# Performance work log

Measured on AMD Instinct MI355X. Metric: run time of the kernel, lower is better.

The kernel has to match this reference:

```python
import jax, jax.numpy as jnp
import numpy as np

N_NODES = 20000
N_EDGES = 320000
NUM_FEATURES = 128
CUTOFF = 5.0
NUM_RBF = 20
EPS = 1e-8


def setup_inputs() -> dict:
    key = jax.random.key(0)
    ks = jax.random.split(key, 10)
    v = jax.random.normal(ks[0], (N_NODES, NUM_FEATURES, 3), dtype=jnp.float32)
    s = jax.random.normal(ks[1], (N_NODES, NUM_FEATURES), dtype=jnp.float32)
    # edge list: col0 = src idx, col1 = dst idx (js), cols 2:5 = displacement vector
    src = jax.random.randint(ks[2], (N_EDGES,), 0, N_NODES).astype(jnp.float32)
    dst = jax.random.randint(ks[3], (N_EDGES,), 0, N_NODES).astype(jnp.float32)
    vec = jax.random.normal(ks[4], (N_EDGES, 3), dtype=jnp.float32) * 2.0
    r = jnp.concatenate([src[:, None], dst[:, None], vec], axis=1)
    # s_path params (torch Linear weight [out,in] -> stored here as [in,out])
    W1 = jax.random.normal(ks[5], (NUM_FEATURES, NUM_FEATURES), dtype=jnp.float32) * np.sqrt(2.0 / NUM_FEATURES)
    b1 = jnp.zeros((NUM_FEATURES,), dtype=jnp.float32)
    W2 = jax.random.normal(ks[6], (NUM_FEATURES, 3 * NUM_FEATURES), dtype=jnp.float32) * np.sqrt(2.0 / NUM_FEATURES)
    b2 = jnp.zeros((3 * NUM_FEATURES,), dtype=jnp.float32)
    # r_path params
    Wr = jax.random.normal(ks[7], (NUM_RBF, 3 * NUM_FEATURES), dtype=jnp.float32) * np.sqrt(1.0 / NUM_RBF)
    br = jnp.zeros((3 * NUM_FEATURES,), dtype=jnp.float32)
    return {"v": v, "s": s, "r": r, "W1": W1, "b1": b1, "W2": W2, "b2": b2, "Wr": Wr, "br": br}


def reference(v, s, r, W1, b1, W2, b2, Wr, br):
    nf = NUM_FEATURES
    js = r[:, 1].astype(jnp.int32)          # [E] destination node indices
    rv = r[:, 2:]                            # [E,3] displacement vectors

    # s_path: Linear -> SiLU -> Linear, computed per-node then gathered
    h = s @ W1 + b1
    phi = (h * jax.nn.sigmoid(h)) @ W2 + b2  # [N, 3*nf]

    # RBF expansion of edge distances
    norm_r = jnp.linalg.norm(rv, axis=1, keepdims=True)          # [E,1]
    norm_c = jnp.clip(norm_r, EPS)
    n = jnp.arange(1, NUM_RBF + 1, dtype=rv.dtype)[None, :]      # [1,20]
    rbf = jnp.clip(jnp.sin(n * (jnp.pi / CUTOFF) * norm_c) / (norm_c + EPS), -1.0, 1.0)

    # r_path Linear then cosine cutoff applied elementwise to the features
    Wf = rbf @ Wr + br                                            # [E, 3*nf]
    Wf = 0.5 * (jnp.cos(jnp.pi * Wf / CUTOFF) + 1.0) * (Wf < CUTOFF).astype(Wf.dtype)

    pre = phi[js, :] * Wf                                         # [E, 3*nf]
    split_1 = pre[:, :nf]
    split_2 = pre[:, nf:2 * nf]
    split_3 = pre[:, 2 * nf:]

    # NOTE: original code divides the normalized vector by the norm again
    rvn = rv / (norm_r + EPS)
    dir_term = rvn / (norm_r + EPS)                               # [E,3]
    left_2 = v[js, :, :] * split_1[:, :, None] + split_3[:, :, None] * dir_term[:, None, :]

    delta_v = jnp.zeros_like(v).at[js].add(left_2)
    delta_s = jnp.zeros_like(s).at[js].add(split_2)
    return (delta_v, delta_s)
```

## Files before the change

kernel.cpp:

```cpp
#include <hip/hip_runtime.h>
#include <math.h>

#define NND 20000
#define NE  320000
#define NF  128
#define NRBF 20
#define DEGCAP 64
#define SCATB 1250

typedef float f32x4 __attribute__((ext_vector_type(4)));
typedef short bf16x8 __attribute__((ext_vector_type(8)));

static constexpr float FCUT = 5.0f;
static constexpr float FEPS = 1e-8f;

__device__ __forceinline__ unsigned short f2bf(float x) {
    unsigned int u = __builtin_bit_cast(unsigned int, x);
    u += 0x7FFFu + ((u >> 16) & 1u);
    return (unsigned short)(u >> 16);
}
__device__ __forceinline__ float bf2f(unsigned short h) {
    unsigned int u = ((unsigned int)h) << 16;
    return __builtin_bit_cast(float, u);
}

__global__ __launch_bounds__(256) void prep_k(const float* __restrict__ r,
                                              int* __restrict__ cursor,
                                              float4* __restrict__ payload,
                                              const float* __restrict__ W1,
                                              const float* __restrict__ W2,
                                              const float* __restrict__ Wr,
                                              const float* __restrict__ br,
                                              unsigned short* __restrict__ Wp1,
                                              unsigned short* __restrict__ Wp2,
                                              unsigned short* __restrict__ WrP) {
    if (blockIdx.x < SCATB) {
        int e = blockIdx.x * 256 + threadIdx.x;
        if (e >= NE) return;
        const float* re = r + (size_t)e * 5;
        int j = (int)re[1];
        float x = re[2], y = re[3], z = re[4];
        float nrm = sqrtf(x * x + y * y + z * z);
        float inv = 1.0f / ((nrm + FEPS) * (nrm + FEPS));
        int pos = atomicAdd(&cursor[j], 1);
        if (pos < DEGCAP)
            payload[((size_t)j << 6) + pos] = make_float4(x * inv, y * inv, z * inv, nrm);
        return;
    }
    int fid = (blockIdx.x - SCATB) * 256 + threadIdx.x;
    if (fid < 2048) {
        int lane = fid & 63, kk = (fid >> 6) & 3, nch = fid >> 8;
        int col = nch * 16 + (lane & 15);
        int k0 = kk * 32 + ((lane >> 4) * 8);
        unsigned short* o = Wp1 + (size_t)fid * 8;
#pragma unroll
        for (int j = 0; j < 8; j++) o[j] = f2bf(W1[(size_t)(k0 + j) * 128 + col]);
    } else if (fid < 2048 + 6144) {
        int f2 = fid - 2048;
        int lane = f2 & 63, kk = (f2 >> 6) & 3, nch = f2 >> 8;
        int col = nch * 16 + (lane & 15);
        int k0 = kk * 32 + ((lane >> 4) * 8);
        unsigned short* o = Wp2 + (size_t)f2 * 8;
#pragma unroll
        for (int j = 0; j < 8; j++) o[j] = f2bf(W2[(size_t)(k0 + j) * 384 + col]);
    } else if (fid < 2048 + 6144 + 1536) {
        int f3 = fid - 8192;
        int lane = f3 & 63, ft = f3 >> 6;
        int col = ft * 16 + (lane & 15);
        int k0 = (lane >> 4) * 8;
        unsigned short* o = WrP + (size_t)f3 * 8;
#pragma unroll
        for (int j = 0; j < 8; j++) {
            int k = k0 + j;
            float val;
            if (k < NRBF)            val = 0.1f * Wr[(size_t)k * 384 + col];
            else if (k == NRBF)      val = 0.1f * br[col];
            else if (k == NRBF + 1)  val = 1.0f;
            else                     val = 0.0f;
            o[j] = f2bf(val);
        }
    }
}

__global__ __launch_bounds__(256) void mlp_k(const float* __restrict__ s,
                                             const unsigned short* __restrict__ Wp1,
                                             const float* __restrict__ b1,
                                             const unsigned short* __restrict__ Wp2,
                                             const float* __restrict__ b2,
                                             unsigned short* __restrict__ phi) {
    __shared__ unsigned short lds[4 * 8192];
    int tid = threadIdx.x;
    int lane = tid & 63, wave = tid >> 6;
    int node0 = blockIdx.x * 64 + wave * 16;
    int arow = lane & 15, kgrp = lane >> 4;
    unsigned short* hW = lds + wave * 8192;
    unsigned short* pW = hW + 2048;

    int anode = node0 + arow; if (anode > NND - 1) anode = NND - 1;
    const float* ap = s + (size_t)anode * NF + kgrp * 8;
    bf16x8 afrag[4];
#pragma unroll
    for (int kk = 0; kk < 4; kk++) {
        float4 x0 = *(const float4*)(ap + kk * 32);
        float4 x1 = *(const float4*)(ap + kk * 32 + 4);
        union { unsigned short u[8]; bf16x8 v; } c;
        c.u[0] = f2bf(x0.x); c.u[1] = f2bf(x0.y); c.u[2] = f2bf(x0.z); c.u[3] = f2bf(x0.w);
        c.u[4] = f2bf(x1.x); c.u[5] = f2bf(x1.y); c.u[6] = f2bf(x1.z); c.u[7] = f2bf(x1.w);
        afrag[kk] = c.v;
    }
    f32x4 acc[8];
#pragma unroll
    for (int n = 0; n < 8; n++) acc[n] = (f32x4)(0.0f);
    const bf16x8* W8a = (const bf16x8*)Wp1;
#pragma unroll
    for (int nch = 0; nch < 8; nch++)
#pragma unroll
        for (int kk = 0; kk < 4; kk++)
            acc[nch] = __builtin_amdgcn_mfma_f32_16x16x32_bf16(
                afrag[kk], W8a[(nch * 4 + kk) * 64 + lane], acc[nch], 0, 0, 0);
#pragma unroll
    for (int nch = 0; nch < 8; nch++) {
        int col = nch * 16 + arow;
        float bb = b1[col];
#pragma unroll
        for (int rg = 0; rg < 4; rg++) {
            int row = kgrp * 4 + rg;
            float x = acc[nch][rg] + bb;
            float y = x / (1.0f + __expf(-x));
            hW[row * 128 + col] = f2bf(y);
        }
    }
    __syncthreads();
    bf16x8 hfrag[4];
#pragma unroll
    for (int kk = 0; kk < 4; kk++)
        hfrag[kk] = *(const bf16x8*)(hW + arow * 128 + kk * 32 + kgrp * 8);
#pragma unroll
    for (int c = 0; c < 3; c++) {
        f32x4 acc2[8];
#pragma unroll
        for (int n = 0; n < 8; n++) acc2[n] = (f32x4)(0.0f);
        const bf16x8* W8b = (const bf16x8*)Wp2;
#pragma unroll
        for (int nch = 0; nch < 8; nch++)
#pragma unroll
            for (int kk = 0; kk < 4; kk++)
                acc2[nch] = __builtin_amdgcn_mfma_f32_16x16x32_bf16(
                    hfrag[kk], W8b[((c * 8 + nch) * 4 + kk) * 64 + lane], acc2[nch], 0, 0, 0);
#pragma unroll
        for (int nch = 0; nch < 8; nch++) {
            int colg = c * 128 + nch * 16 + arow;
            float bb = b2[colg];
#pragma unroll
            for (int rg = 0; rg < 4; rg++) {
                int row = kgrp * 4 + rg;
                pW[row * 384 + colg] = f2bf(acc2[nch][rg] + bb);
            }
        }
    }
    __syncthreads();
#pragma unroll
    for (int it = 0; it < 12; it++) {
        int idx = it * 64 + lane;
        int row = idx / 48, ch = idx - row * 48;
        int node = node0 + row;
        if (node < NND) {
            uint4 val = *(const uint4*)(pW + row * 384 + ch * 8);
            *(uint4*)(phi + (size_t)node * 384 + ch * 8) = val;
        }
    }
}

__global__ __launch_bounds__(256) void reduce7_k(const int* __restrict__ cursor,
                                                 const float4* __restrict__ payload,
                                                 const unsigned short* __restrict__ phi,
                                                 const float* __restrict__ v,
                                                 const unsigned short* __restrict__ WrP,
                                                 float* __restrict__ dv,
                                                 float* __restrict__ ds) {
    int tid = threadIdx.x;
    int lane = tid & 63;
    int la = lane & 15, kg = lane >> 4;
    int gwid = blockIdx.x * 4 + (tid >> 6);
    int w = gwid & 1;
    int jstart = gwid >> 1;
    int jstride = (gridDim.x * 4) >> 1;

    bool isKg2 = (kg == 2), isKg3 = (kg == 3);

    bf16x8 wrf[12];
#pragma unroll
    for (int q = 0; q < 12; q++)
        wrf[q] = *(const bf16x8*)(WrP + (size_t)(((2 * q + w) << 6) + lane) * 8);

    for (int j = jstart; j < NND; j += jstride) {
        int deg = cursor[j]; if (deg > DEGCAP) deg = DEGCAP;
        const float4* pay = payload + ((size_t)j << 6);

        int f = (2 * kg + w) * 16 + la;
        const unsigned short* ph = phi + (size_t)j * 384;
        float p1 = bf2f(ph[f]), p2 = bf2f(ph[128 + f]), p3 = bf2f(ph[256 + f]);
        size_t vb = ((size_t)j * NF + f) * 3;
        float vx = v[vb], vy = v[vb + 1], vz = v[vb + 2];

        float a0[4], a1[4], sdx[4], sdy[4], sdz[4];
        float DX = 0.f, DY = 0.f, DZ = 0.f;
#pragma unroll
        for (int i = 0; i < 4; i++) { a0[i] = 0.f; a1[i] = 0.f; sdx[i] = 0.f; sdy[i] = 0.f; sdz[i] = 0.f; }

        int ntiles = (deg + 15) >> 4;
        float4 p_next;
        if (deg > 0) p_next = pay[la < deg ? la : deg - 1];

        for (int t5 = 0; t5 < ntiles; t5++) {
            float4 p = p_next;
            if (t5 + 1 < ntiles) {
                int idx = (t5 + 1) * 16 + la;
                p_next = pay[idx < deg ? idx : deg - 1];
            }
            int cnt = deg - t5 * 16; if (cnt > 16) cnt = 16;

            float nc = fmaxf(p.w, FEPS);
            float invd = 1.0f / (nc + FEPS);
            float sv[8];
#pragma unroll
            for (int j2 = 0; j2 < 8; j2++) {
                int k = kg * 8 + j2;
                float s0 = __builtin_amdgcn_sinf((float)(k + 1) * 0.1f * nc) * invd;
                sv[j2] = fminf(fmaxf(s0, -1.f), 1.f);
            }
            unsigned int w0, w1, w2, w3;
            asm("v_cvt_pk_bf16_f32 %0, %1, %2" : "=v"(w0) : "v"(sv[0]), "v"(sv[1]));
            asm("v_cvt_pk_bf16_f32 %0, %1, %2" : "=v"(w1) : "v"(sv[2]), "v"(sv[3]));
            asm("v_cvt_pk_bf16_f32 %0, %1, %2" : "=v"(w2) : "v"(sv[4]), "v"(sv[5]));
            asm("v_cvt_pk_bf16_f32 %0, %1, %2" : "=v"(w3) : "v"(sv[6]), "v"(sv[7]));
            w2 = isKg2 ? ((la < cnt) ? 0x00003F80u : 0x41203F80u) : w2;
            w0 = isKg3 ? 0u : w0;
            w1 = isKg3 ? 0u : w1;
            w2 = isKg3 ? 0u : w2;
            w3 = (kg >= 2) ? 0u : w3;
            union { unsigned int wrd[4]; bf16x8 v8; } af;
            af.wrd[0] = w0; af.wrd[1] = w1; af.wrd[2] = w2; af.wrd[3] = w3;

            float dx[4], dy[4], dz[4];
#pragma unroll
            for (int rr = 0; rr < 4; rr++) {
                int er = kg * 4 + rr;
                dx[rr] = __shfl(p.x, er);
                dy[rr] = __shfl(p.y, er);
                dz[rr] = __shfl(p.z, er);
            }
            DX += dx[0] + dx[1] + dx[2] + dx[3];
            DY += dy[0] + dy[1] + dy[2] + dy[3];
            DZ += dz[0] + dz[1] + dz[2] + dz[3];

#pragma unroll
            for (int q = 0; q < 12; q++) {
                f32x4 d = __builtin_amdgcn_mfma_f32_16x16x32_bf16(
                    af.v8, wrf[q], (f32x4)(0.0f), 0, 0, 0);
#pragma unroll
                for (int rr = 0; rr < 4; rr++) {
                    float t = __builtin_amdgcn_cosf(fminf(d[rr], 0.5f));
                    if (q < 4)      a0[q] += t;
                    else if (q < 8) a1[q - 4] += t;
                    else {
                        sdx[q - 8] = fmaf(t, dx[rr], sdx[q - 8]);
                        sdy[q - 8] = fmaf(t, dy[rr], sdy[q - 8]);
                        sdz[q - 8] = fmaf(t, dz[rr], sdz[q - 8]);
                    }
                }
            }
        }
#pragma unroll
        for (int i = 0; i < 4; i++) {
            a0[i] += __shfl_xor(a0[i], 16);  a0[i] += __shfl_xor(a0[i], 32);
            a1[i] += __shfl_xor(a1[i], 16);  a1[i] += __shfl_xor(a1[i], 32);
            sdx[i] += __shfl_xor(sdx[i], 16); sdx[i] += __shfl_xor(sdx[i], 32);
            sdy[i] += __shfl_xor(sdy[i], 16); sdy[i] += __shfl_xor(sdy[i], 32);
            sdz[i] += __shfl_xor(sdz[i], 16); sdz[i] += __shfl_xor(sdz[i], 32);
        }
        DX += __shfl_xor(DX, 16); DX += __shfl_xor(DX, 32);
        DY += __shfl_xor(DY, 16); DY += __shfl_xor(DY, 32);
        DZ += __shfl_xor(DZ, 16); DZ += __shfl_xor(DZ, 32);
        float R = (float)(((deg + 15) >> 4) << 4);

        float A0 = 0, A1 = 0, SX = 0, SY = 0, SZ = 0;
#pragma unroll
        for (int i = 0; i < 4; i++) {
            if (kg == i) { A0 = a0[i]; A1 = a1[i]; SX = sdx[i]; SY = sdy[i]; SZ = sdz[i]; }
        }
        float sum1 = 0.5f * (A0 + R);
        float sum2 = 0.5f * (A1 + R);
        float sx = 0.5f * (SX + DX);
        float sy = 0.5f * (SY + DY);
        float sz = 0.5f * (SZ + DZ);

        ds[(size_t)j * NF + f] = p2 * sum2;
        float c1 = p1 * sum1;
        dv[vb + 0] = fmaf(vx, c1, p3 * sx);
        dv[vb + 1] = fmaf(vy, c1, p3 * sy);
        dv[vb + 2] = fmaf(vz, c1, p3 * sz);
    }
}

extern "C" void kernel_launch(void* const* d_in, const int* in_sizes, int n_in,
                              void* d_out, int out_size, void* d_ws, size_t ws_size,
                              hipStream_t stream) {
    const float* v  = (const float*)d_in[0];
    const float* s  = (const float*)d_in[1];
    const float* r  = (const float*)d_in[2];
    const float* W1 = (const float*)d_in[3];
    const float* b1 = (const float*)d_in[4];
    const float* W2 = (const float*)d_in[5];
    const float* b2 = (const float*)d_in[6];
    const float* Wr = (const float*)d_in[7];
    const float* br = (const float*)d_in[8];

    float* dv = (float*)d_out;
    float* ds = dv + (size_t)NND * NF * 3;

    char* ws = (char*)d_ws;
    int* cursor             = (int*)ws;
    float* payload          = (float*)(ws + 80128);
    unsigned short* Wp1     = (unsigned short*)(ws + 20560128);
    unsigned short* Wp2     = (unsigned short*)(ws + 20592896);
    unsigned short* WrP     = (unsigned short*)(ws + 20691200);
    unsigned short* phi     = (unsigned short*)(ws + 20715776);

    hipMemsetAsync(cursor, 0, NND * sizeof(int), stream);
    prep_k<<<SCATB + 38, 256, 0, stream>>>(r, cursor, (float4*)payload,
                                           W1, W2, Wr, br, Wp1, Wp2, WrP);

    mlp_k<<<(NND + 63) / 64, 256, 0, stream>>>(s, Wp1, b1, Wp2, b2, phi);

    reduce7_k<<<2560, 256, 0, stream>>>(cursor, (const float4*)payload, phi, v, WrP, dv, ds);
}
```

Measured before the change: 109.7 us.

## Process two destination nodes per wave to interleave independent MFMA/transcendental chains

```diff
diff --git a/kernel.cpp b/kernel.cpp
--- a/kernel.cpp
+++ b/kernel.cpp
@@ -171,7 +171,63 @@
     }
 }
 
-__global__ __launch_bounds__(256) void reduce7_k(const int* __restrict__ cursor,
+__device__ __forceinline__ void tile_body(float4 p, int cnt, int la, int kg,
+                                          bool isKg2, bool isKg3,
+                                          const bf16x8* __restrict__ wrf,
+                                          float* __restrict__ a0, float* __restrict__ a1,
+                                          float* __restrict__ sdx, float* __restrict__ sdy,
+                                          float* __restrict__ sdz,
+                                          float& PX, float& PY, float& PZ) {
+    float nc = fmaxf(p.w, FEPS);
+    float invd = 1.0f / (nc + FEPS);
+    float sv[8];
+#pragma unroll
+    for (int j2 = 0; j2 < 8; j2++) {
+        int k = kg * 8 + j2;
+        float s0 = __builtin_amdgcn_sinf((float)(k + 1) * 0.1f * nc) * invd;
+        sv[j2] = fminf(fmaxf(s0, -1.f), 1.f);
+    }
+    unsigned int w0, w1, w2, w3;
+    asm("v_cvt_pk_bf16_f32 %0, %1, %2" : "=v"(w0) : "v"(sv[0]), "v"(sv[1]));
+    asm("v_cvt_pk_bf16_f32 %0, %1, %2" : "=v"(w1) : "v"(sv[2]), "v"(sv[3]));
+    asm("v_cvt_pk_bf16_f32 %0, %1, %2" : "=v"(w2) : "v"(sv[4]), "v"(sv[5]));
+    asm("v_cvt_pk_bf16_f32 %0, %1, %2" : "=v"(w3) : "v"(sv[6]), "v"(sv[7]));
+    w2 = isKg2 ? ((la < cnt) ? 0x00003F80u : 0x41203F80u) : w2;
+    w0 = isKg3 ? 0u : w0;
+    w1 = isKg3 ? 0u : w1;
+    w2 = isKg3 ? 0u : w2;
+    w3 = (kg >= 2) ? 0u : w3;
+    union { unsigned int wrd[4]; bf16x8 v8; } af;
+    af.wrd[0] = w0; af.wrd[1] = w1; af.wrd[2] = w2; af.wrd[3] = w3;
+
+    PX += p.x; PY += p.y; PZ += p.z;
+
+    float dx[4], dy[4], dz[4];
+#pragma unroll
+    for (int rr = 0; rr < 4; rr++) {
+        int er = kg * 4 + rr;
+        dx[rr] = __shfl(p.x, er);
+        dy[rr] = __shfl(p.y, er);
+        dz[rr] = __shfl(p.z, er);
+    }
+#pragma unroll
+    for (int q = 0; q < 12; q++) {
+        f32x4 d = __builtin_amdgcn_mfma_f32_16x16x32_bf16(af.v8, wrf[q], (f32x4)(0.0f), 0, 0, 0);
+#pragma unroll
+        for (int rr = 0; rr < 4; rr++) {
+            float t = __builtin_amdgcn_cosf(fminf(d[rr], 0.5f));
+            if (q < 4)      a0[q] += t;
+            else if (q < 8) a1[q - 4] += t;
+            else {
+                sdx[q - 8] = fmaf(t, dx[rr], sdx[q - 8]);
+                sdy[q - 8] = fmaf(t, dy[rr], sdy[q - 8]);
+                sdz[q - 8] = fmaf(t, dz[rr], sdz[q - 8]);
+            }
+        }
+    }
+}
+
+__global__ __launch_bounds__(256) void reduce9_k(const int* __restrict__ cursor,
                                                  const float4* __restrict__ payload,
                                                  const unsigned short* __restrict__ phi,
                                                  const float* __restrict__ v,
@@ -183,8 +239,8 @@
     int la = lane & 15, kg = lane >> 4;
     int gwid = blockIdx.x * 4 + (tid >> 6);
     int w = gwid & 1;
-    int jstart = gwid >> 1;
-    int jstride = (gridDim.x * 4) >> 1;
+    int pstart = gwid >> 1;
+    int pstride = (gridDim.x * 4) >> 1;
 
     bool isKg2 = (kg == 2), isKg3 = (kg == 3);
 
@@ -193,113 +249,112 @@
     for (int q = 0; q < 12; q++)
         wrf[q] = *(const bf16x8*)(WrP + (size_t)(((2 * q + w) << 6) + lane) * 8);
 
-    for (int j = jstart; j < NND; j += jstride) {
-        int deg = cursor[j]; if (deg > DEGCAP) deg = DEGCAP;
-        const float4* pay = payload + ((size_t)j << 6);
+    for (int pr = pstart; pr < NND / 2; pr += pstride) {
+        int jA = 2 * pr, jB = 2 * pr + 1;
+        int degA = cursor[jA]; if (degA > DEGCAP) degA = DEGCAP;
+        int degB = cursor[jB]; if (degB > DEGCAP) degB = DEGCAP;
+        const float4* payA = payload + ((size_t)jA << 6);
+        const float4* payB = payload + ((size_t)jB << 6);
 
         int f = (2 * kg + w) * 16 + la;
-        const unsigned short* ph = phi + (size_t)j * 384;
-        float p1 = bf2f(ph[f]), p2 = bf2f(ph[128 + f]), p3 = bf2f(ph[256 + f]);
-        size_t vb = ((size_t)j * NF + f) * 3;
-        float vx = v[vb], vy = v[vb + 1], vz = v[vb + 2];
-
-        float a0[4], a1[4], sdx[4], sdy[4], sdz[4];
-        float DX = 0.f, DY = 0.f, DZ = 0.f;
-#pragma unroll
-        for (int i = 0; i < 4; i++) { a0[i] = 0.f; a1[i] = 0.f; sdx[i] = 0.f; sdy[i] = 0.f; sdz[i] = 0.f; }
-
-        int ntiles = (deg + 15) >> 4;
-        float4 p_next;
-        if (deg > 0) p_next = pay[la < deg ? la : deg - 1];
-
-        for (int t5 = 0; t5 < ntiles; t5++) {
-            float4 p = p_next;
-            if (t5 + 1 < ntiles) {
-                int idx = (t5 + 1) * 16 + la;
-                p_next = pay[idx < deg ? idx : deg - 1];
+        const unsigned short* phA = phi + (size_t)jA * 384;
+        const unsigned short* phB = phi + (size_t)jB * 384;
+        float p1A = bf2f(phA[f]), p2A = bf2f(phA[128 + f]), p3A = bf2f(phA[256 + f]);
+        float p1B = bf2f(phB[f]), p2B = bf2f(phB[128 + f]), p3B = bf2f(phB[256 + f]);
+        size_t vbA = ((size_t)jA * NF + f) * 3;
+        size_t vbB = ((size_t)jB * NF + f) * 3;
+        float vxA = v[vbA], vyA = v[vbA + 1], vzA = v[vbA + 2];
+        float vxB = v[vbB], vyB = v[vbB + 1], vzB = v[vbB + 2];
+
+        float a0A[4], a1A[4], sdxA[4], sdyA[4], sdzA[4];
+        float a0B[4], a1B[4], sdxB[4], sdyB[4], sdzB[4];
+#pragma unroll
+        for (int i = 0; i < 4; i++) {
+            a0A[i] = 0.f; a1A[i] = 0.f; sdxA[i] = 0.f; sdyA[i] = 0.f; sdzA[i] = 0.f;
+            a0B[i] = 0.f; a1B[i] = 0.f; sdxB[i] = 0.f; sdyB[i] = 0.f; sdzB[i] = 0.f;
+        }
+        float PXA = 0.f, PYA = 0.f, PZA = 0.f;
+        float PXB = 0.f, PYB = 0.f, PZB = 0.f;
+
+        int ntA = (degA + 15) >> 4, ntB = (degB + 15) >> 4;
+        int ntMin = ntA < ntB ? ntA : ntB;
+
+        for (int t5 = 0; t5 < ntMin; t5++) {
+            int ia = t5 * 16 + la;
+            float4 pA = payA[ia < degA ? ia : degA - 1];
+            float4 pB = payB[ia < degB ? ia : degB - 1];
+            int cntA = degA - t5 * 16; if (cntA > 16) cntA = 16;
+            int cntB = degB - t5 * 16; if (cntB > 16) cntB = 16;
+            tile_body(pA, cntA, la, kg, isKg2, isKg3, wrf, a0A, a1A, sdxA, sdyA, sdzA, PXA, PYA, PZA);
+            tile_body(pB, cntB, la, kg, isKg2, isKg3, wrf, a0B, a1B, sdxB, sdyB, sdzB, PXB, PYB, PZB);
+        }
+        for (int t5 = ntMin; t5 < ntA; t5++) {
+            int ia = t5 * 16 + la;
+            float4 pA = payA[ia < degA ? ia : degA - 1];
+            int cntA = degA - t5 * 16; if (cntA > 16) cntA = 16;
+            tile_body(pA, cntA, la, kg, isKg2, isKg3, wrf, a0A, a1A, sdxA, sdyA, sdzA, PXA, PYA, PZA);
+        }
+        for (int t5 = ntMin; t5 < ntB; t5++) {
+            int ib = t5 * 16 + la;
+            float4 pB = payB[ib < degB ? ib : degB - 1];
+            int cntB = degB - t5 * 16; if (cntB > 16) cntB = 16;
+            tile_body(pB, cntB, la, kg, isKg2, isKg3, wrf, a0B, a1B, sdxB, sdyB, sdzB, PXB, PYB, PZB);
+        }
+
+#pragma unroll
+        for (int i = 0; i < 4; i++) {
+            a0A[i] += __shfl_xor(a0A[i], 16);  a0A[i] += __shfl_xor(a0A[i], 32);
+            a1A[i] += __shfl_xor(a1A[i], 16);  a1A[i] += __shfl_xor(a1A[i], 32);
+            sdxA[i] += __shfl_xor(sdxA[i], 16); sdxA[i] += __shfl_xor(sdxA[i], 32);
+            sdyA[i] += __shfl_xor(sdyA[i], 16); sdyA[i] += __shfl_xor(sdyA[i], 32);
+            sdzA[i] += __shfl_xor(sdzA[i], 16); sdzA[i] += __shfl_xor(sdzA[i], 32);
+            a0B[i] += __shfl_xor(a0B[i], 16);  a0B[i] += __shfl_xor(a0B[i], 32);
+            a1B[i] += __shfl_xor(a1B[i], 16);  a1B[i] += __shfl_xor(a1B[i], 32);
+            sdxB[i] += __shfl_xor(sdxB[i], 16); sdxB[i] += __shfl_xor(sdxB[i], 32);
+            sdyB[i] += __shfl_xor(sdyB[i], 16); sdyB[i] += __shfl_xor(sdyB[i], 32);
+            sdzB[i] += __shfl_xor(sdzB[i], 16); sdzB[i] += __shfl_xor(sdzB[i], 32);
+        }
+#pragma unroll
+        for (int m = 1; m < 16; m <<= 1) {
+            PXA += __shfl_xor(PXA, m); PYA += __shfl_xor(PYA, m); PZA += __shfl_xor(PZA, m);
+            PXB += __shfl_xor(PXB, m); PYB += __shfl_xor(PYB, m); PZB += __shfl_xor(PZB, m);
+        }
+        float RA = (float)(ntA << 4);
+        float RB = (float)(ntB << 4);
+
+        float A0A = 0, A1A = 0, SXA = 0, SYA = 0, SZA = 0;
+        float A0B = 0, A1B = 0, SXB = 0, SYB = 0, SZB = 0;
+#pragma unroll
+        for (int i = 0; i < 4; i++) {
+            if (kg == i) {
+                A0A = a0A[i]; A1A = a1A[i]; SXA = sdxA[i]; SYA = sdyA[i]; SZA = sdzA[i];
+                A0B = a0B[i]; A1B = a1B[i]; SXB = sdxB[i]; SYB = sdyB[i]; SZB = sdzB[i];
             }
-            int cnt = deg - t5 * 16; if (cnt > 16) cnt = 16;
-
-            float nc = fmaxf(p.w, FEPS);
-            float invd = 1.0f / (nc + FEPS);
-            float sv[8];
-#pragma unroll
-            for (int j2 = 0; j2 < 8; j2++) {
-                int k = kg * 8 + j2;
-                float s0 = __builtin_amdgcn_sinf((float)(k + 1) * 0.1f * nc) * invd;
-                sv[j2] = fminf(fmaxf(s0, -1.f), 1.f);
-            }
-            unsigned int w0, w1, w2, w3;
-            asm("v_cvt_pk_bf16_f32 %0, %1, %2" : "=v"(w0) : "v"(sv[0]), "v"(sv[1]));
-            asm("v_cvt_pk_bf16_f32 %0, %1, %2" : "=v"(w1) : "v"(sv[2]), "v"(sv[3]));
-            asm("v_cvt_pk_bf16_f32 %0, %1, %2" : "=v"(w2) : "v"(sv[4]), "v"(sv[5]));
-            asm("v_cvt_pk_bf16_f32 %0, %1, %2" : "=v"(w3) : "v"(sv[6]), "v"(sv[7]));
-            w2 = isKg2 ? ((la < cnt) ? 0x00003F80u : 0x41203F80u) : w2;
-            w0 = isKg3 ? 0u : w0;
-            w1 = isKg3 ? 0u : w1;
-            w2 = isKg3 ? 0u : w2;
-            w3 = (kg >= 2) ? 0u : w3;
-            union { unsigned int wrd[4]; bf16x8 v8; } af;
-            af.wrd[0] = w0; af.wrd[1] = w1; af.wrd[2] = w2; af.wrd[3] = w3;
-
-            float dx[4], dy[4], dz[4];
-#pragma unroll
-            for (int rr = 0; rr < 4; rr++) {
-                int er = kg * 4 + rr;
-                dx[rr] = __shfl(p.x, er);
-                dy[rr] = __shfl(p.y, er);
-                dz[rr] = __shfl(p.z, er);
-            }
-            DX += dx[0] + dx[1] + dx[2] + dx[3];
-            DY += dy[0] + dy[1] + dy[2] + dy[3];
-            DZ += dz[0] + dz[1] + dz[2] + dz[3];
-
-#pragma unroll
-            for (int q = 0; q < 12; q++) {
-                f32x4 d = __builtin_amdgcn_mfma_f32_16x16x32_bf16(
-                    af.v8, wrf[q], (f32x4)(0.0f), 0, 0, 0);
-#pragma unroll
-                for (int rr = 0; rr < 4; rr++) {
-                    float t = __builtin_amdgcn_cosf(fminf(d[rr], 0.5f));
-                    if (q < 4)      a0[q] += t;
-                    else if (q < 8) a1[q - 4] += t;
-                    else {
-                        sdx[q - 8] = fmaf(t, dx[rr], sdx[q - 8]);
-                        sdy[q - 8] = fmaf(t, dy[rr], sdy[q - 8]);
-                        sdz[q - 8] = fmaf(t, dz[rr], sdz[q - 8]);
-                    }
-                }
-            }
-        }
-#pragma unroll
-        for (int i = 0; i < 4; i++) {
-            a0[i] += __shfl_xor(a0[i], 16);  a0[i] += __shfl_xor(a0[i], 32);
-            a1[i] += __shfl_xor(a1[i], 16);  a1[i] += __shfl_xor(a1[i], 32);
-            sdx[i] += __shfl_xor(sdx[i], 16); sdx[i] += __shfl_xor(sdx[i], 32);
-            sdy[i] += __shfl_xor(sdy[i], 16); sdy[i] += __shfl_xor(sdy[i], 32);
-            sdz[i] += __shfl_xor(sdz[i], 16); sdz[i] += __shfl_xor(sdz[i], 32);
-        }
-        DX += __shfl_xor(DX, 16); DX += __shfl_xor(DX, 32);
-        DY += __shfl_xor(DY, 16); DY += __shfl_xor(DY, 32);
-        DZ += __shfl_xor(DZ, 16); DZ += __shfl_xor(DZ, 32);
-        float R = (float)(((deg + 15) >> 4) << 4);
-
-        float A0 = 0, A1 = 0, SX = 0, SY = 0, SZ = 0;
-#pragma unroll
-        for (int i = 0; i < 4; i++) {
-            if (kg == i) { A0 = a0[i]; A1 = a1[i]; SX = sdx[i]; SY = sdy[i]; SZ = sdz[i]; }
-        }
-        float sum1 = 0.5f * (A0 + R);
-        float sum2 = 0.5f * (A1 + R);
-        float sx = 0.5f * (SX + DX);
-        float sy = 0.5f * (SY + DY);
-        float sz = 0.5f * (SZ + DZ);
-
-        ds[(size_t)j * NF + f] = p2 * sum2;
-        float c1 = p1 * sum1;
-        dv[vb + 0] = fmaf(vx, c1, p3 * sx);
-        dv[vb + 1] = fmaf(vy, c1, p3 * sy);
-        dv[vb + 2] = fmaf(vz, c1, p3 * sz);
+        }
+        {
+            float sum1 = 0.5f * (A0A + RA);
+            float sum2 = 0.5f * (A1A + RA);
+            float sx = 0.5f * (SXA + PXA);
+            float sy = 0.5f * (SYA + PYA);
+            float sz = 0.5f * (SZA + PZA);
+            ds[(size_t)jA * NF + f] = p2A * sum2;
+            float c1 = p1A * sum1;
+            dv[vbA + 0] = fmaf(vxA, c1, p3A * sx);
+            dv[vbA + 1] = fmaf(vyA, c1, p3A * sy);
+            dv[vbA + 2] = fmaf(vzA, c1, p3A * sz);
+        }
+        {
+            float sum1 = 0.5f * (A0B + RB);
+            float sum2 = 0.5f * (A1B + RB);
+            float sx = 0.5f * (SXB + PXB);
+            float sy = 0.5f * (SYB + PYB);
+            float sz = 0.5f * (SZB + PZB);
+            ds[(size_t)jB * NF + f] = p2B * sum2;
+            float c1 = p1B * sum1;
+            dv[vbB + 0] = fmaf(vxB, c1, p3B * sx);
+            dv[vbB + 1] = fmaf(vyB, c1, p3B * sy);
+            dv[vbB + 2] = fmaf(vzB, c1, p3B * sz);
+        }
     }
 }
 
@@ -333,5 +388,5 @@
 
     mlp_k<<<(NND + 63) / 64, 256, 0, stream>>>(s, Wp1, b1, Wp2, b2, phi);
 
-    reduce7_k<<<2560, 256, 0, stream>>>(cursor, (const float4*)payload, phi, v, WrP, dv, ds);
-}
+    reduce9_k<<<2560, 256, 0, stream>>>(cursor, (const float4*)payload, phi, v, WrP, dv, ds);
+}
```

Result: slower. 147.3 us (+34.3%).

## Replace capped per-node edge buckets with CSR layout and precomputed RBF records

Applied to the files above, without the earlier changes.

```diff
diff --git a/kernel.cpp b/kernel.cpp
--- a/kernel.cpp
+++ b/kernel.cpp
@@ -5,13 +5,11 @@
 #define NE  320000
 #define NF  128
 #define NRBF 20
-#define DEGCAP 64
-#define SCATB 1250
+#define HISTB 1250
 
 typedef float f32x4 __attribute__((ext_vector_type(4)));
 typedef short bf16x8 __attribute__((ext_vector_type(8)));
 
-static constexpr float FCUT = 5.0f;
 static constexpr float FEPS = 1e-8f;
 
 __device__ __forceinline__ unsigned short f2bf(float x) {
@@ -24,30 +22,24 @@
     return __builtin_bit_cast(float, u);
 }
 
-__global__ __launch_bounds__(256) void prep_k(const float* __restrict__ r,
-                                              int* __restrict__ cursor,
-                                              float4* __restrict__ payload,
-                                              const float* __restrict__ W1,
-                                              const float* __restrict__ W2,
-                                              const float* __restrict__ Wr,
-                                              const float* __restrict__ br,
-                                              unsigned short* __restrict__ Wp1,
-                                              unsigned short* __restrict__ Wp2,
-                                              unsigned short* __restrict__ WrP) {
-    if (blockIdx.x < SCATB) {
+__global__ __launch_bounds__(256) void histpack_k(const float* __restrict__ r,
+                                                  int* __restrict__ counts,
+                                                  const float* __restrict__ W1,
+                                                  const float* __restrict__ W2,
+                                                  const float* __restrict__ Wr,
+                                                  const float* __restrict__ br,
+                                                  unsigned short* __restrict__ Wp1,
+                                                  unsigned short* __restrict__ Wp2,
+                                                  unsigned short* __restrict__ WrP) {
+    if (blockIdx.x < HISTB) {
         int e = blockIdx.x * 256 + threadIdx.x;
-        if (e >= NE) return;
-        const float* re = r + (size_t)e * 5;
-        int j = (int)re[1];
-        float x = re[2], y = re[3], z = re[4];
-        float nrm = sqrtf(x * x + y * y + z * z);
-        float inv = 1.0f / ((nrm + FEPS) * (nrm + FEPS));
-        int pos = atomicAdd(&cursor[j], 1);
-        if (pos < DEGCAP)
-            payload[((size_t)j << 6) + pos] = make_float4(x * inv, y * inv, z * inv, nrm);
+        if (e < NE) {
+            int j = (int)r[(size_t)e * 5 + 1];
+            atomicAdd(&counts[j], 1);
+        }
         return;
     }
-    int fid = (blockIdx.x - SCATB) * 256 + threadIdx.x;
+    int fid = (blockIdx.x - HISTB) * 256 + threadIdx.x;
     if (fid < 2048) {
         int lane = fid & 63, kk = (fid >> 6) & 3, nch = fid >> 8;
         int col = nch * 16 + (lane & 15);
@@ -80,6 +72,72 @@
             o[j] = f2bf(val);
         }
     }
+}
+
+__global__ __launch_bounds__(1024) void scan_k(int* counts_cursor,
+                                               int* offsets) {
+    __shared__ int part[1024];
+    const int CH = 20;
+    int t = threadIdx.x;
+    int base = t * CH;
+    int loc[CH];
+    int sum = 0;
+#pragma unroll
+    for (int i = 0; i < CH; i++) {
+        int idx = base + i;
+        int c = (idx < NND) ? counts_cursor[idx] : 0;
+        loc[i] = sum;
+        sum += c;
+    }
+    part[t] = sum;
+    __syncthreads();
+    for (int off = 1; off < 1024; off <<= 1) {
+        int val = (t >= off) ? part[t - off] : 0;
+        __syncthreads();
+        part[t] += val;
+        __syncthreads();
+    }
+    int excl = part[t] - sum;
+#pragma unroll
+    for (int i = 0; i < CH; i++) {
+        int idx = base + i;
+        if (idx < NND) {
+            int o = excl + loc[i];
+            offsets[idx] = o;
+            counts_cursor[idx] = o;
+        }
+    }
+    if (t == 1023) offsets[NND] = part[1023];
+}
+
+__global__ __launch_bounds__(256) void scatrec_k(const float* __restrict__ r,
+                                                 int* __restrict__ cursor,
+                                                 unsigned short* __restrict__ rec) {
+    int e = blockIdx.x * 256 + threadIdx.x;
+    if (e >= NE) return;
+    const float* re = r + (size_t)e * 5;
+    int j = (int)re[1];
+    float x = re[2], y = re[3], z = re[4];
+    float nrm = sqrtf(x * x + y * y + z * z);
+    float nc = fmaxf(nrm, FEPS);
+    float invd = 1.0f / (nc + FEPS);
+    float inv2 = 1.0f / ((nrm + FEPS) * (nrm + FEPS));
+    unsigned short rb[24];
+#pragma unroll
+    for (int k = 0; k < NRBF; k++) {
+        float s0 = __builtin_amdgcn_sinf((float)(k + 1) * 0.1f * nc) * invd;
+        rb[k] = f2bf(fminf(fmaxf(s0, -1.f), 1.f));
+    }
+    rb[20] = f2bf(x * inv2);
+    rb[21] = f2bf(y * inv2);
+    rb[22] = f2bf(z * inv2);
+    rb[23] = 0;
+    int pos = atomicAdd(&cursor[j], 1);
+    uint4* dst = (uint4*)(rec + (size_t)pos * 24);
+    const uint4* src = (const uint4*)rb;
+    dst[0] = src[0];
+    dst[1] = src[1];
+    dst[2] = src[2];
 }
 
 __global__ __launch_bounds__(256) void mlp_k(const float* __restrict__ s,
@@ -171,13 +229,13 @@
     }
 }
 
-__global__ __launch_bounds__(256) void reduce7_k(const int* __restrict__ cursor,
-                                                 const float4* __restrict__ payload,
-                                                 const unsigned short* __restrict__ phi,
-                                                 const float* __restrict__ v,
-                                                 const unsigned short* __restrict__ WrP,
-                                                 float* __restrict__ dv,
-                                                 float* __restrict__ ds) {
+__global__ __launch_bounds__(256) void reduce10_k(const int* __restrict__ offsets,
+                                                  const unsigned short* __restrict__ rec,
+                                                  const unsigned short* __restrict__ phi,
+                                                  const float* __restrict__ v,
+                                                  const unsigned short* __restrict__ WrP,
+                                                  float* __restrict__ dv,
+                                                  float* __restrict__ ds) {
     int tid = threadIdx.x;
     int lane = tid & 63;
     int la = lane & 15, kg = lane >> 4;
@@ -194,8 +252,8 @@
         wrf[q] = *(const bf16x8*)(WrP + (size_t)(((2 * q + w) << 6) + lane) * 8);
 
     for (int j = jstart; j < NND; j += jstride) {
-        int deg = cursor[j]; if (deg > DEGCAP) deg = DEGCAP;
-        const float4* pay = payload + ((size_t)j << 6);
+        int beg = offsets[j], end = offsets[j + 1];
+        int deg = end - beg;
 
         int f = (2 * kg + w) * 16 + la;
         const unsigned short* ph = phi + (size_t)j * 384;
@@ -209,46 +267,38 @@
         for (int i = 0; i < 4; i++) { a0[i] = 0.f; a1[i] = 0.f; sdx[i] = 0.f; sdy[i] = 0.f; sdz[i] = 0.f; }
 
         int ntiles = (deg + 15) >> 4;
-        float4 p_next;
-        if (deg > 0) p_next = pay[la < deg ? la : deg - 1];
+        uint4 c_next = make_uint4(0, 0, 0, 0);
+        if (ntiles > 0 && !isKg3) {
+            int idx = beg + (la < deg ? la : deg - 1);
+            c_next = *(const uint4*)(rec + (size_t)idx * 24 + kg * 8);
+        }
 
         for (int t5 = 0; t5 < ntiles; t5++) {
-            float4 p = p_next;
-            if (t5 + 1 < ntiles) {
-                int idx = (t5 + 1) * 16 + la;
-                p_next = pay[idx < deg ? idx : deg - 1];
+            uint4 c = c_next;
+            if (t5 + 1 < ntiles && !isKg3) {
+                int i2 = t5 * 16 + 16 + la;
+                int idx = beg + (i2 < deg ? i2 : deg - 1);
+                c_next = *(const uint4*)(rec + (size_t)idx * 24 + kg * 8);
             }
             int cnt = deg - t5 * 16; if (cnt > 16) cnt = 16;
 
-            float nc = fmaxf(p.w, FEPS);
-            float invd = 1.0f / (nc + FEPS);
-            float sv[8];
-#pragma unroll
-            for (int j2 = 0; j2 < 8; j2++) {
-                int k = kg * 8 + j2;
-                float s0 = __builtin_amdgcn_sinf((float)(k + 1) * 0.1f * nc) * invd;
-                sv[j2] = fminf(fmaxf(s0, -1.f), 1.f);
-            }
-            unsigned int w0, w1, w2, w3;
-            asm("v_cvt_pk_bf16_f32 %0, %1, %2" : "=v"(w0) : "v"(sv[0]), "v"(sv[1]));
-            asm("v_cvt_pk_bf16_f32 %0, %1, %2" : "=v"(w1) : "v"(sv[2]), "v"(sv[3]));
-            asm("v_cvt_pk_bf16_f32 %0, %1, %2" : "=v"(w2) : "v"(sv[4]), "v"(sv[5]));
-            asm("v_cvt_pk_bf16_f32 %0, %1, %2" : "=v"(w3) : "v"(sv[6]), "v"(sv[7]));
-            w2 = isKg2 ? ((la < cnt) ? 0x00003F80u : 0x41203F80u) : w2;
-            w0 = isKg3 ? 0u : w0;
-            w1 = isKg3 ? 0u : w1;
-            w2 = isKg3 ? 0u : w2;
-            w3 = (kg >= 2) ? 0u : w3;
-            union { unsigned int wrd[4]; bf16x8 v8; } af;
-            af.wrd[0] = w0; af.wrd[1] = w1; af.wrd[2] = w2; af.wrd[3] = w3;
+            float dirx = bf2f((unsigned short)(c.z & 0xFFFF));
+            float diry = bf2f((unsigned short)(c.z >> 16));
+            float dirz = bf2f((unsigned short)(c.w & 0xFFFF));
+            if (isKg2) {
+                c.z = (la < cnt) ? 0x00003F80u : 0x41203F80u;
+                c.w = 0u;
+            }
+            union { uint4 u; bf16x8 v8; } af;
+            af.u = c;
 
             float dx[4], dy[4], dz[4];
 #pragma unroll
             for (int rr = 0; rr < 4; rr++) {
                 int er = kg * 4 + rr;
-                dx[rr] = __shfl(p.x, er);
-                dy[rr] = __shfl(p.y, er);
-                dz[rr] = __shfl(p.z, er);
+                dx[rr] = __shfl(dirx, 32 + er);
+                dy[rr] = __shfl(diry, 32 + er);
+                dz[rr] = __shfl(dirz, 32 + er);
             }
             DX += dx[0] + dx[1] + dx[2] + dx[3];
             DY += dy[0] + dy[1] + dy[2] + dy[3];
@@ -282,7 +332,7 @@
         DX += __shfl_xor(DX, 16); DX += __shfl_xor(DX, 32);
         DY += __shfl_xor(DY, 16); DY += __shfl_xor(DY, 32);
         DZ += __shfl_xor(DZ, 16); DZ += __shfl_xor(DZ, 32);
-        float R = (float)(((deg + 15) >> 4) << 4);
+        float R = (float)(ntiles << 4);
 
         float A0 = 0, A1 = 0, SX = 0, SY = 0, SZ = 0;
 #pragma unroll
@@ -320,18 +370,20 @@
     float* ds = dv + (size_t)NND * NF * 3;
 
     char* ws = (char*)d_ws;
-    int* cursor             = (int*)ws;
-    float* payload          = (float*)(ws + 80128);
-    unsigned short* Wp1     = (unsigned short*)(ws + 20560128);
-    unsigned short* Wp2     = (unsigned short*)(ws + 20592896);
-    unsigned short* WrP     = (unsigned short*)(ws + 20691200);
-    unsigned short* phi     = (unsigned short*)(ws + 20715776);
+    int* offsets            = (int*)ws;
+    int* cursor             = (int*)(ws + 80128);
+    unsigned short* rec     = (unsigned short*)(ws + 160256);
+    unsigned short* Wp1     = (unsigned short*)(ws + 15520256);
+    unsigned short* Wp2     = (unsigned short*)(ws + 15553024);
+    unsigned short* WrP     = (unsigned short*)(ws + 15651328);
+    unsigned short* phi     = (unsigned short*)(ws + 15675904);
 
     hipMemsetAsync(cursor, 0, NND * sizeof(int), stream);
-    prep_k<<<SCATB + 38, 256, 0, stream>>>(r, cursor, (float4*)payload,
-                                           W1, W2, Wr, br, Wp1, Wp2, WrP);
+    histpack_k<<<HISTB + 38, 256, 0, stream>>>(r, cursor, W1, W2, Wr, br, Wp1, Wp2, WrP);
+    scan_k<<<1, 1024, 0, stream>>>(cursor, offsets);
+    scatrec_k<<<(NE + 255) / 256, 256, 0, stream>>>(r, cursor, rec);
 
     mlp_k<<<(NND + 63) / 64, 256, 0, stream>>>(s, Wp1, b1, Wp2, b2, phi);
 
-    reduce7_k<<<2560, 256, 0, stream>>>(cursor, (const float4*)payload, phi, v, WrP, dv, ds);
-}
+    reduce10_k<<<2560, 256, 0, stream>>>(offsets, rec, phi, v, WrP, dv, ds);
+}
```

Result: slower. 145.4 us (+32.5%).
